# Performance work log

Hardware: AMD Instinct MI355X
Metric: run time of the kernel (lower is better)

## Reference

```python
import jax, jax.numpy as jnp
import numpy as np
import math

B, S, D = 4, 2048, 1024
H, DK, DV = 16, 64, 64
EPS = 1e-5
SCALE = math.sqrt(1.0 / D)  # NOTE: original scales by 1/sqrt(d_model), not 1/sqrt(d_k)


def setup_inputs() -> dict:
    key = jax.random.key(0)
    ks = jax.random.split(key, 12)
    s = 0.02
    return {
        "Q": jax.random.normal(ks[0], (B, S, D), jnp.float32),
        "K": jax.random.normal(ks[1], (B, S, D), jnp.float32),
        "V": jax.random.normal(ks[2], (B, S, D), jnp.float32),
        # stacked per-head projection weights (torch Linear: y = x @ W.T + b)
        "Wq": jax.random.normal(ks[3], (H, D, DK), jnp.float32) * s,
        "bq": jnp.zeros((H, DK), jnp.float32),
        "Wk": jax.random.normal(ks[4], (H, D, DK), jnp.float32) * s,
        "bk": jnp.zeros((H, DK), jnp.float32),
        "Wv": jax.random.normal(ks[5], (H, D, DV), jnp.float32) * s,
        "bv": jnp.zeros((H, DV), jnp.float32),
        "Wo": jax.random.normal(ks[6], (H * DV, D), jnp.float32) * s,
        "bo": jnp.zeros((D,), jnp.float32),
        "gamma": jnp.ones((D,), jnp.float32),
        "beta": jnp.zeros((D,), jnp.float32),
    }


def reference(Q, K, V, Wq, bq, Wk, bk, Wv, bv, Wo, bo, gamma, beta):
    residual = Q
    # batched per-head projections: [B,S,D] x [H,D,dk] -> [B,H,S,dk]
    q = jnp.einsum("bsd,hdk->bhsk", Q, Wq) + bq[None, :, None, :]
    k = jnp.einsum("bsd,hdk->bhsk", K, Wk) + bk[None, :, None, :]
    v = jnp.einsum("bsd,hdv->bhsv", V, Wv) + bv[None, :, None, :]
    # scaled dot-product attention (scale uses d_model, per original code)
    attn = jax.nn.softmax(jnp.einsum("bhsk,bhtk->bhst", q, k) * SCALE, axis=-1)
    out = jnp.einsum("bhst,bhtv->bhsv", attn, v)  # [B,H,S,DV]
    # concat heads along feature dim: [B,S,H*DV]
    out = out.transpose(0, 2, 1, 3).reshape(B, S, H * DV)
    out = out @ Wo + bo  # output projection
    # dropout is identity in eval mode
    out = out + residual
    # BatchNorm1d over (B,S) per channel (training-mode batch stats)
    mean = jnp.mean(out, axis=(0, 1))
    var = jnp.mean(jnp.square(out - mean), axis=(0, 1))
    out = (out - mean) * jax.lax.rsqrt(var + EPS) * gamma + beta
    return out.transpose(0, 2, 1)  # (B, d_model, S)
```

## Files before the change

kernel.cpp:

```cpp
#include <hip/hip_runtime.h>

#define B_ 4
#define S_ 2048
#define D_ 1024
#define H_ 16
#define SCALE_ 0.03125f
#define EPS_ 1e-5f
#define NBS_ 8192

typedef unsigned short ushort_t;
typedef __attribute__((ext_vector_type(8))) short short8;
typedef __attribute__((ext_vector_type(4))) short short4v;
typedef __attribute__((ext_vector_type(4))) float floatx4;

__device__ __forceinline__ ushort_t f2bf(float f) {
  union { float f; unsigned u; } v; v.f = f;
  unsigned r = v.u + 0x7fffu + ((v.u >> 16) & 1u);
  return (ushort_t)(r >> 16);
}

__device__ __forceinline__ float fast_exp2(float x) {
#if __has_builtin(__builtin_amdgcn_exp2f)
  return __builtin_amdgcn_exp2f(x);
#else
  return __expf(x * 0.6931471805599453f);
#endif
}

__device__ __forceinline__ short8 cvt8(float4 a, float4 b) {
  short8 r;
  r[0] = (short)f2bf(a.x); r[1] = (short)f2bf(a.y);
  r[2] = (short)f2bf(a.z); r[3] = (short)f2bf(a.w);
  r[4] = (short)f2bf(b.x); r[5] = (short)f2bf(b.y);
  r[6] = (short)f2bf(b.z); r[7] = (short)f2bf(b.w);
  return r;
}

__device__ __forceinline__ void gload16(const void* g, void* l) {
  __builtin_amdgcn_global_load_lds(
      (const __attribute__((address_space(1))) unsigned int*)g,
      (__attribute__((address_space(3))) unsigned int*)l, 16, 0, 0);
}

__global__ __launch_bounds__(256) void cvtx_k(const float* __restrict__ src,
                                              ushort_t* __restrict__ dst)
{
  size_t i = ((size_t)blockIdx.x * 256 + threadIdx.x) * 8;
  float4 a = *(const float4*)(src + i);
  float4 b = *(const float4*)(src + i + 4);
  *(short8*)(dst + i) = cvt8(a, b);
}

__global__ __launch_bounds__(256) void wtr_k(const float* __restrict__ src,
                                             ushort_t* __restrict__ dst, int mode)
{
  __shared__ float t[64][65];
  const int tr = blockIdx.x, tc = blockIdx.y;
  const float* sb; int sld;
  if (mode == 0) { sb = src + (size_t)tr * 65536 + (size_t)tc * 64 * 64; sld = 64; }
  else           { sb = src + (size_t)tc * 64 * 1024 + (size_t)tr * 64;  sld = 1024; }
  const int tid = threadIdx.x;
  const int rr = tid >> 2, cs = (tid & 3) * 16;
  const float* p = sb + (size_t)rr * sld + cs;
#pragma unroll
  for (int j = 0; j < 16; ++j) t[rr][cs + j] = p[j];
  __syncthreads();
  ushort_t* dp = dst + (size_t)(tr * 64 + rr) * 1024 + tc * 64 + cs;
#pragma unroll
  for (int j = 0; j < 16; ++j) dp[j] = f2bf(t[cs + j][rr]);
}

__global__ __launch_bounds__(256) void gemm_proj(
    const ushort_t* __restrict__ A, const ushort_t* __restrict__ Bw,
    const float* __restrict__ bias, ushort_t* __restrict__ outp, float scale)
{
  __shared__ ushort_t As[128 * 32];
  __shared__ ushort_t Bs[128 * 32];
  const int tid = threadIdx.x;
  const int wv = tid >> 6, lane = tid & 63, quad = lane >> 4, l16 = lane & 15;
  const int m0 = blockIdx.x * 128, n0 = blockIdx.y * 128;
  const int wm = wv & 1, wn = wv >> 1;
  const int lrow = lane >> 2, lkc = (lane & 3) * 8;

  floatx4 acc[4][4];
#pragma unroll
  for (int i = 0; i < 4; ++i)
#pragma unroll
    for (int j = 0; j < 4; ++j) acc[i][j] = (floatx4){0.f, 0.f, 0.f, 0.f};

  for (int k0 = 0; k0 < 1024; k0 += 32) {
    __syncthreads();
#pragma unroll
    for (int j = 0; j < 2; ++j) {
      const int rb = wv * 32 + j * 16;
      gload16(A + (size_t)(m0 + rb + lrow) * 1024 + k0 + lkc, (char*)As + rb * 64);
      gload16(Bw + (size_t)(n0 + rb + lrow) * 1024 + k0 + lkc, (char*)Bs + rb * 64);
    }
    __syncthreads();
    short8 af[4], bf[4];
#pragma unroll
    for (int i = 0; i < 4; ++i)
      af[i] = *(const short8*)&As[(wm * 64 + i * 16 + l16) * 32 + quad * 8];
#pragma unroll
    for (int i = 0; i < 4; ++i)
      bf[i] = *(const short8*)&Bs[(wn * 64 + i * 16 + l16) * 32 + quad * 8];
#pragma unroll
    for (int mi = 0; mi < 4; ++mi)
#pragma unroll
      for (int ni = 0; ni < 4; ++ni)
        acc[mi][ni] = __builtin_amdgcn_mfma_f32_16x16x32_bf16(
            af[mi], bf[ni], acc[mi][ni], 0, 0, 0);
  }

  const int b = m0 >> 11;
  const int sbase = (m0 & 2047) + wm * 64;
#pragma unroll
  for (int ni = 0; ni < 4; ++ni) {
    const int c = n0 + wn * 64 + ni * 16 + l16;
    const int h = c >> 6, nn = c & 63;
    const float bs = bias[c];
    ushort_t* op = outp + (size_t)(b * 16 + h) * 2048 * 64 + nn;
#pragma unroll
    for (int mi = 0; mi < 4; ++mi)
#pragma unroll
      for (int r = 0; r < 4; ++r) {
        int s = sbase + mi * 16 + quad * 4 + r;
        op[(size_t)s * 64] = f2bf((acc[mi][ni][r] + bs) * scale);
      }
  }
}

__global__ __launch_bounds__(256) void gemm_projT(
    const ushort_t* __restrict__ A, const ushort_t* __restrict__ Bw,
    const float* __restrict__ bias, ushort_t* __restrict__ outp)
{
  __shared__ ushort_t As[128 * 32];
  __shared__ ushort_t Bs[128 * 32];
  const int tid = threadIdx.x;
  const int wv = tid >> 6, lane = tid & 63, quad = lane >> 4, l16 = lane & 15;
  const int m0 = blockIdx.x * 128, n0 = blockIdx.y * 128;
  const int wm = wv & 1, wn = wv >> 1;
  const int lrow = lane >> 2, lkc = (lane & 3) * 8;

  floatx4 acc[4][4];
#pragma unroll
  for (int i = 0; i < 4; ++i)
#pragma unroll
    for (int j = 0; j < 4; ++j) acc[i][j] = (floatx4){0.f, 0.f, 0.f, 0.f};

  for (int k0 = 0; k0 < 1024; k0 += 32) {
    __syncthreads();
#pragma unroll
    for (int j = 0; j < 2; ++j) {
      const int rb = wv * 32 + j * 16;
      gload16(A + (size_t)(m0 + rb + lrow) * 1024 + k0 + lkc, (char*)As + rb * 64);
      gload16(Bw + (size_t)(n0 + rb + lrow) * 1024 + k0 + lkc, (char*)Bs + rb * 64);
    }
    __syncthreads();
    short8 af[4], bf[4];
#pragma unroll
    for (int i = 0; i < 4; ++i)
      af[i] = *(const short8*)&As[(wm * 64 + i * 16 + l16) * 32 + quad * 8];
#pragma unroll
    for (int i = 0; i < 4; ++i)
      bf[i] = *(const short8*)&Bs[(wn * 64 + i * 16 + l16) * 32 + quad * 8];
#pragma unroll
    for (int mi = 0; mi < 4; ++mi)
#pragma unroll
      for (int ni = 0; ni < 4; ++ni)
        acc[mi][ni] = __builtin_amdgcn_mfma_f32_16x16x32_bf16(
            af[mi], bf[ni], acc[mi][ni], 0, 0, 0);
  }

  const int b = m0 >> 11;
  const int sbase = (m0 & 2047) + wm * 64;
#pragma unroll
  for (int ni = 0; ni < 4; ++ni) {
    const int c = n0 + wn * 64 + ni * 16 + l16;
    const int h = c >> 6, nn = c & 63;
    const float bs = bias[c];
    ushort_t* op = outp + ((size_t)(b * 16 + h) * 64 + nn) * 2048;
#pragma unroll
    for (int mi = 0; mi < 4; ++mi) {
      int s0v = sbase + mi * 16 + quad * 4;
      short4v p;
#pragma unroll
      for (int r = 0; r < 4; ++r) p[r] = (short)f2bf(acc[mi][ni][r] + bs);
      *(short4v*)(op + s0v) = p;
    }
  }
}

__global__ __launch_bounds__(256) void gemm_oproj(
    const ushort_t* __restrict__ A, const ushort_t* __restrict__ Bw,
    const float* __restrict__ bo, const float* __restrict__ resid,
    float* __restrict__ y)
{
  __shared__ ushort_t As[128 * 32];
  __shared__ ushort_t Bs[128 * 32];
  const int tid = threadIdx.x;
  const int wv = tid >> 6, lane = tid & 63, quad = lane >> 4, l16 = lane & 15;
  const int m0 = blockIdx.x * 128, n0 = blockIdx.y * 128;
  const int wm = wv & 1, wn = wv >> 1;
  const int lrow = lane >> 2, lkc = (lane & 3) * 8;

  floatx4 acc[4][4];
#pragma unroll
  for (int i = 0; i < 4; ++i)
#pragma unroll
    for (int j = 0; j < 4; ++j) acc[i][j] = (floatx4){0.f, 0.f, 0.f, 0.f};

  for (int k0 = 0; k0 < 1024; k0 += 32) {
    __syncthreads();
#pragma unroll
    for (int j = 0; j < 2; ++j) {
      const int rb = wv * 32 + j * 16;
      gload16(A + (size_t)(m0 + rb + lrow) * 1024 + k0 + lkc, (char*)As + rb * 64);
      gload16(Bw + (size_t)(n0 + rb + lrow) * 1024 + k0 + lkc, (char*)Bs + rb * 64);
    }
    __syncthreads();
    short8 af[4], bf[4];
#pragma unroll
    for (int i = 0; i < 4; ++i)
      af[i] = *(const short8*)&As[(wm * 64 + i * 16 + l16) * 32 + quad * 8];
#pragma unroll
    for (int i = 0; i < 4; ++i)
      bf[i] = *(const short8*)&Bs[(wn * 64 + i * 16 + l16) * 32 + quad * 8];
#pragma unroll
    for (int mi = 0; mi < 4; ++mi)
#pragma unroll
      for (int ni = 0; ni < 4; ++ni)
        acc[mi][ni] = __builtin_amdgcn_mfma_f32_16x16x32_bf16(
            af[mi], bf[ni], acc[mi][ni], 0, 0, 0);
  }

  const int mb = m0 + wm * 64;
#pragma unroll
  for (int ni = 0; ni < 4; ++ni) {
    const int d = n0 + wn * 64 + ni * 16 + l16;
    const float bs = bo[d];
#pragma unroll
    for (int mi = 0; mi < 4; ++mi)
#pragma unroll
      for (int r = 0; r < 4; ++r) {
        int m = mb + mi * 16 + quad * 4 + r;
        y[(size_t)m * 1024 + d] = acc[mi][ni][r] + bs + resid[(size_t)m * 1024 + d];
      }
  }
}

__global__ __launch_bounds__(256, 4) void attn_k(
    const ushort_t* __restrict__ q, const ushort_t* __restrict__ k,
    const ushort_t* __restrict__ vt, ushort_t* __restrict__ ao)
{
  __shared__ ushort_t lds[20480];
  const int tid = threadIdx.x;
  const int wv = tid >> 6, lane = tid & 63, quad = lane >> 4, l16 = lane & 15;
  const int q0 = blockIdx.x * 128, h = blockIdx.y, b = blockIdx.z;
  const size_t bh = (size_t)(b * H_ + h) * S_;
  const ushort_t* vb = vt + (size_t)(b * H_ + h) * 64 * S_;

  short8 aq[2][2];
#pragma unroll
  for (int rb = 0; rb < 2; ++rb) {
    const ushort_t* qrow = q + (bh + q0 + wv * 32 + rb * 16 + l16) * 64;
    aq[rb][0] = *(const short8*)(qrow + quad * 8);
    aq[rb][1] = *(const short8*)(qrow + 32 + quad * 8);
  }

  floatx4 o[2][4];
  float ll[2][4];
#pragma unroll
  for (int rb = 0; rb < 2; ++rb) {
#pragma unroll
    for (int cb = 0; cb < 4; ++cb) o[rb][cb] = (floatx4){0.f, 0.f, 0.f, 0.f};
#pragma unroll
    for (int r = 0; r < 4; ++r) ll[rb][r] = 0.f;
  }

  const int pbase = 16384 + wv * 1024 + (l16 >> 3) * 128 + quad * 32 + (l16 & 7);

  auto stage = [&](int nb, int t0) {
#pragma unroll
    for (int i = 0; i < 4; ++i) {
      const int idx = wv * 4 + i;
      const int cb = (idx >> 1) & 3, hf = idx & 1;
      if (idx < 8)
        gload16(k + (bh + t0 + cb * 16 + l16) * 64 + hf * 32 + quad * 8,
                (char*)lds + nb * 8192 + idx * 1024);
      else
        gload16(vb + (size_t)(cb * 16 + l16) * S_ + t0 + hf * 32 + quad * 8,
                (char*)lds + 16384 + nb * 8192 + (idx - 8) * 1024);
    }
  };

  stage(0, 0);
  asm volatile("s_waitcnt vmcnt(0)" ::: "memory");
  __syncthreads();

  for (int t0 = 0; t0 < S_; t0 += 64) {
    const int nb = (t0 >> 6) & 1;
    const ushort_t* KsC = lds + nb * 4096;
    const ushort_t* VsC = lds + 8192 + nb * 4096;
    if (t0 + 64 < S_) stage(nb ^ 1, t0 + 64);

    floatx4 sc[2][4];
#pragma unroll
    for (int rb = 0; rb < 2; ++rb)
#pragma unroll
      for (int cb = 0; cb < 4; ++cb) sc[rb][cb] = (floatx4){0.f, 0.f, 0.f, 0.f};
#pragma unroll
    for (int hf = 0; hf < 2; ++hf) {
      short8 bk[4];
#pragma unroll
      for (int cb = 0; cb < 4; ++cb)
        bk[cb] = *(const short8*)&KsC[(cb * 2 + hf) * 512 + lane * 8];
#pragma unroll
      for (int rb = 0; rb < 2; ++rb)
#pragma unroll
        for (int cb = 0; cb < 4; ++cb)
          sc[rb][cb] = __builtin_amdgcn_mfma_f32_16x16x32_bf16(
              aq[rb][hf], bk[cb], sc[rb][cb], 0, 0, 0);
    }

#pragma unroll
    for (int rb = 0; rb < 2; ++rb) {
#pragma unroll
      for (int cb = 0; cb < 4; ++cb)
#pragma unroll
        for (int r = 0; r < 4; ++r) {
          float p = fast_exp2(sc[rb][cb][r]);
          ll[rb][r] += p;
          lds[pbase + (cb >> 1) * 512 + (cb & 1) * 256 + r * 8] = f2bf(p);
        }
      asm volatile("s_waitcnt lgkmcnt(0)" ::: "memory");
      __builtin_amdgcn_wave_barrier();
#pragma unroll
      for (int hf = 0; hf < 2; ++hf) {
        short8 ap = *(const short8*)&lds[16384 + wv * 1024 + hf * 512 + lane * 8];
        short8 bvf[4];
#pragma unroll
        for (int cb = 0; cb < 4; ++cb)
          bvf[cb] = *(const short8*)&VsC[(cb * 2 + hf) * 512 + lane * 8];
#pragma unroll
        for (int cb = 0; cb < 4; ++cb)
          o[rb][cb] = __builtin_amdgcn_mfma_f32_16x16x32_bf16(
              ap, bvf[cb], o[rb][cb], 0, 0, 0);
      }
      asm volatile("s_waitcnt lgkmcnt(0)" ::: "memory");
      __builtin_amdgcn_wave_barrier();
    }

    asm volatile("s_waitcnt vmcnt(0)" ::: "memory");
    __syncthreads();
  }

#pragma unroll
  for (int rb = 0; rb < 2; ++rb)
#pragma unroll
    for (int r = 0; r < 4; ++r) {
#pragma unroll
      for (int off = 8; off >= 1; off >>= 1)
        ll[rb][r] += __shfl_xor(ll[rb][r], off);
      ll[rb][r] = 1.f / ll[rb][r];
    }
#pragma unroll
  for (int rb = 0; rb < 2; ++rb)
#pragma unroll
    for (int cb = 0; cb < 4; ++cb)
#pragma unroll
      for (int r = 0; r < 4; ++r) {
        float val = o[rb][cb][r] * ll[rb][r];
        size_t idx = (size_t)(b * S_ + q0 + wv * 32 + rb * 16 + quad * 4 + r) * 1024
                     + h * 64 + cb * 16 + l16;
        ao[idx] = f2bf(val);
      }
}

__global__ __launch_bounds__(256) void stats_k(
    const float* __restrict__ y, float* __restrict__ s1, float* __restrict__ s2)
{
  const int tid = threadIdx.x;
  const int r0 = blockIdx.x * 32;
  float a[4] = {0.f, 0.f, 0.f, 0.f}, bb[4] = {0.f, 0.f, 0.f, 0.f};
  for (int r = 0; r < 32; ++r) {
    const float* row = y + (size_t)(r0 + r) * D_;
#pragma unroll
    for (int j = 0; j < 4; ++j) {
      float vv = row[tid + j * 256];
      a[j] += vv;
      bb[j] += vv * vv;
    }
  }
#pragma unroll
  for (int j = 0; j < 4; ++j) {
    atomicAdd(&s1[tid + j * 256], a[j]);
    atomicAdd(&s2[tid + j * 256], bb[j]);
  }
}

__global__ __launch_bounds__(256) void norm_k(
    const float* __restrict__ y, const float* __restrict__ s1,
    const float* __restrict__ s2, const float* __restrict__ gamma,
    const float* __restrict__ beta, float* __restrict__ out)
{
  __shared__ float tile[64][65];
  __shared__ float scl[64], sft[64];
  const int tid = threadIdx.x;
  const int s0 = blockIdx.x * 64, d0 = blockIdx.y * 64, b = blockIdx.z;

  if (tid < 64) {
    int d = d0 + tid;
    float mean = s1[d] * (1.f / (float)NBS_);
    float var = s2[d] * (1.f / (float)NBS_) - mean * mean;
    float rstd = rsqrtf(var + EPS_);
    float g = gamma[d];
    scl[tid] = rstd * g;
    sft[tid] = beta[d] - mean * rstd * g;
  }
  __syncthreads();

  const int si = tid >> 2, dc = (tid & 3) * 16;
  const float* row = y + (size_t)(b * S_ + s0 + si) * D_ + d0 + dc;
#pragma unroll
  for (int j = 0; j < 16; ++j)
    tile[si][dc + j] = row[j] * scl[dc + j] + sft[dc + j];
  __syncthreads();

  const int di = tid >> 2, sg = (tid & 3) * 16;
  float* dst = out + (size_t)(b * D_ + d0 + di) * S_ + s0 + sg;
#pragma unroll
  for (int jj = 0; jj < 4; ++jj) {
    float4 p;
    p.x = tile[sg + jj * 4 + 0][di];
    p.y = tile[sg + jj * 4 + 1][di];
    p.z = tile[sg + jj * 4 + 2][di];
    p.w = tile[sg + jj * 4 + 3][di];
    *(float4*)(dst + jj * 4) = p;
  }
}

extern "C" void kernel_launch(void* const* d_in, const int* in_sizes, int n_in,
                              void* d_out, int out_size, void* d_ws, size_t ws_size,
                              hipStream_t stream)
{
  (void)in_sizes; (void)n_in; (void)out_size; (void)ws_size;
  const float* Q     = (const float*)d_in[0];
  const float* Kin   = (const float*)d_in[1];
  const float* Vin   = (const float*)d_in[2];
  const float* Wq    = (const float*)d_in[3];
  const float* bq    = (const float*)d_in[4];
  const float* Wk    = (const float*)d_in[5];
  const float* bk    = (const float*)d_in[6];
  const float* Wv    = (const float*)d_in[7];
  const float* bv    = (const float*)d_in[8];
  const float* Wo    = (const float*)d_in[9];
  const float* bo    = (const float*)d_in[10];
  const float* gamma = (const float*)d_in[11];
  const float* beta  = (const float*)d_in[12];
  float* out = (float*)d_out;

  char* ws = (char*)d_ws;
  const size_t MB = 1u << 20;
  ushort_t* xb  = (ushort_t*)(ws);
  ushort_t* wtq = (ushort_t*)(ws + 16 * MB);
  ushort_t* wtk = (ushort_t*)(ws + 18 * MB);
  ushort_t* wtv = (ushort_t*)(ws + 20 * MB);
  ushort_t* wto = (ushort_t*)(ws + 22 * MB);
  ushort_t* qb  = (ushort_t*)(ws + 24 * MB);
  ushort_t* kb  = (ushort_t*)(ws + 40 * MB);
  ushort_t* vtb = (ushort_t*)(ws + 56 * MB);
  ushort_t* ao  = (ushort_t*)(ws);
  float*    y   = (float*)(ws + 24 * MB);
  float*    s1  = (float*)(ws + 56 * MB);
  float*    s2  = (float*)(ws + 56 * MB + 4096);

  wtr_k<<<dim3(16, 16), 256, 0, stream>>>(Wq, wtq, 0);
  wtr_k<<<dim3(16, 16), 256, 0, stream>>>(Wk, wtk, 0);
  wtr_k<<<dim3(16, 16), 256, 0, stream>>>(Wv, wtv, 0);
  wtr_k<<<dim3(16, 16), 256, 0, stream>>>(Wo, wto, 1);

  const float QSC = SCALE_ * 1.44269504088896f;
  cvtx_k<<<4096, 256, 0, stream>>>(Q, xb);
  gemm_proj<<<dim3(64, 8), 256, 0, stream>>>(xb, wtq, bq, qb, QSC);
  cvtx_k<<<4096, 256, 0, stream>>>(Kin, xb);
  gemm_proj<<<dim3(64, 8), 256, 0, stream>>>(xb, wtk, bk, kb, 1.0f);
  cvtx_k<<<4096, 256, 0, stream>>>(Vin, xb);
  gemm_projT<<<dim3(64, 8), 256, 0, stream>>>(xb, wtv, bv, vtb);

  attn_k<<<dim3(16, 16, 4), 256, 0, stream>>>(qb, kb, vtb, ao);
  gemm_oproj<<<dim3(64, 8), 256, 0, stream>>>(ao, wto, bo, Q, y);

  hipMemsetAsync(ws + 56 * MB, 0, 8192, stream);
  stats_k<<<256, 256, 0, stream>>>(y, s1, s2);
  norm_k<<<dim3(32, 16, 4), 256, 0, stream>>>(y, s1, s2, gamma, beta, out);
}
```

Measured before the change: 458.9 us.

## Transpose QK MFMA to write P as packed swizzled rows and hoist V fragment loads

The score MFMA now swaps its operands, so each lane holds four consecutive key columns of one query row. Those probabilities are packed into one 8-byte LDS store per tile, into an XOR-swizzled per-wave P buffer, instead of scattered 2-byte stores. This cuts LDS store count and bank conflicts, and makes the row sum a per-lane accumulation with a cheaper final reduction. V fragments are loaded once per tile for both row blocks, setprio is raised around the MFMA phases, and the intermediate wave barriers are removed. LDS grows and the occupancy hint drops from 4 to 3 blocks.

```diff
diff --git a/kernel.cpp b/kernel.cpp
--- a/kernel.cpp
+++ b/kernel.cpp
@@ -12,6 +12,7 @@
 typedef __attribute__((ext_vector_type(8))) short short8;
 typedef __attribute__((ext_vector_type(4))) short short4v;
 typedef __attribute__((ext_vector_type(4))) float floatx4;
+typedef __attribute__((ext_vector_type(2))) unsigned int uint2v;
 
 __device__ __forceinline__ ushort_t f2bf(float f) {
   union { float f; unsigned u; } v; v.f = f;
@@ -249,11 +250,12 @@
   }
 }
 
-__global__ __launch_bounds__(256, 4) void attn_k(
+__global__ __launch_bounds__(256, 3) void attn_k(
     const ushort_t* __restrict__ q, const ushort_t* __restrict__ k,
     const ushort_t* __restrict__ vt, ushort_t* __restrict__ ao)
 {
-  __shared__ ushort_t lds[20480];
+  __shared__ ushort_t lds[24576];
+  char* ldsb = (char*)lds;
   const int tid = threadIdx.x;
   const int wv = tid >> 6, lane = tid & 63, quad = lane >> 4, l16 = lane & 15;
   const int q0 = blockIdx.x * 128, h = blockIdx.y, b = blockIdx.z;
@@ -269,16 +271,15 @@
   }
 
   floatx4 o[2][4];
-  float ll[2][4];
-#pragma unroll
-  for (int rb = 0; rb < 2; ++rb) {
+  float ll[2] = {0.f, 0.f};
+#pragma unroll
+  for (int rb = 0; rb < 2; ++rb)
 #pragma unroll
     for (int cb = 0; cb < 4; ++cb) o[rb][cb] = (floatx4){0.f, 0.f, 0.f, 0.f};
-#pragma unroll
-    for (int r = 0; r < 4; ++r) ll[rb][r] = 0.f;
-  }
-
-  const int pbase = 16384 + wv * 1024 + (l16 >> 3) * 128 + quad * 32 + (l16 & 7);
+
+  const int swz = (l16 & 7) << 4;
+  const int q8 = quad * 8;
+  const int pb = 32768 + wv * 4096 + l16 * 128;
 
   auto stage = [&](int nb, int t0) {
 #pragma unroll
@@ -309,6 +310,7 @@
     for (int rb = 0; rb < 2; ++rb)
 #pragma unroll
       for (int cb = 0; cb < 4; ++cb) sc[rb][cb] = (floatx4){0.f, 0.f, 0.f, 0.f};
+    __builtin_amdgcn_s_setprio(1);
 #pragma unroll
     for (int hf = 0; hf < 2; ++hf) {
       short8 bk[4];
@@ -320,57 +322,71 @@
 #pragma unroll
         for (int cb = 0; cb < 4; ++cb)
           sc[rb][cb] = __builtin_amdgcn_mfma_f32_16x16x32_bf16(
-              aq[rb][hf], bk[cb], sc[rb][cb], 0, 0, 0);
-    }
+              bk[cb], aq[rb][hf], sc[rb][cb], 0, 0, 0);
+    }
+    __builtin_amdgcn_s_setprio(0);
+
+    short8 bvf[2][4];
+#pragma unroll
+    for (int hf = 0; hf < 2; ++hf)
+#pragma unroll
+      for (int cb = 0; cb < 4; ++cb)
+        bvf[hf][cb] = *(const short8*)&VsC[(cb * 2 + hf) * 512 + lane * 8];
 
 #pragma unroll
     for (int rb = 0; rb < 2; ++rb) {
 #pragma unroll
-      for (int cb = 0; cb < 4; ++cb)
-#pragma unroll
-        for (int r = 0; r < 4; ++r) {
-          float p = fast_exp2(sc[rb][cb][r]);
-          ll[rb][r] += p;
-          lds[pbase + (cb >> 1) * 512 + (cb & 1) * 256 + r * 8] = f2bf(p);
-        }
-      asm volatile("s_waitcnt lgkmcnt(0)" ::: "memory");
-      __builtin_amdgcn_wave_barrier();
+      for (int cb = 0; cb < 4; ++cb) {
+        float p0 = fast_exp2(sc[rb][cb][0]);
+        float p1 = fast_exp2(sc[rb][cb][1]);
+        float p2 = fast_exp2(sc[rb][cb][2]);
+        float p3 = fast_exp2(sc[rb][cb][3]);
+        ll[rb] += (p0 + p1) + (p2 + p3);
+        uint2v w;
+        w[0] = (unsigned)f2bf(p0) | ((unsigned)f2bf(p1) << 16);
+        w[1] = (unsigned)f2bf(p2) | ((unsigned)f2bf(p3) << 16);
+        *(uint2v*)(ldsb + pb + rb * 2048 + ((cb * 32 + q8) ^ swz)) = w;
+      }
+    }
+    asm volatile("s_waitcnt lgkmcnt(0)" ::: "memory");
+    __builtin_amdgcn_sched_barrier(0);
+
+    __builtin_amdgcn_s_setprio(1);
+#pragma unroll
+    for (int rb = 0; rb < 2; ++rb)
 #pragma unroll
       for (int hf = 0; hf < 2; ++hf) {
-        short8 ap = *(const short8*)&lds[16384 + wv * 1024 + hf * 512 + lane * 8];
-        short8 bvf[4];
-#pragma unroll
-        for (int cb = 0; cb < 4; ++cb)
-          bvf[cb] = *(const short8*)&VsC[(cb * 2 + hf) * 512 + lane * 8];
+        short8 ap = *(const short8*)(ldsb + pb + rb * 2048 +
+                                     ((hf * 64 + quad * 16) ^ swz));
 #pragma unroll
         for (int cb = 0; cb < 4; ++cb)
           o[rb][cb] = __builtin_amdgcn_mfma_f32_16x16x32_bf16(
-              ap, bvf[cb], o[rb][cb], 0, 0, 0);
+              ap, bvf[hf][cb], o[rb][cb], 0, 0, 0);
       }
-      asm volatile("s_waitcnt lgkmcnt(0)" ::: "memory");
-      __builtin_amdgcn_wave_barrier();
-    }
+    __builtin_amdgcn_s_setprio(0);
 
     asm volatile("s_waitcnt vmcnt(0)" ::: "memory");
     __syncthreads();
   }
 
 #pragma unroll
+  for (int rb = 0; rb < 2; ++rb) {
+    ll[rb] += __shfl_xor(ll[rb], 16);
+    ll[rb] += __shfl_xor(ll[rb], 32);
+  }
+  float linv[2][4];
+#pragma unroll
   for (int rb = 0; rb < 2; ++rb)
 #pragma unroll
-    for (int r = 0; r < 4; ++r) {
-#pragma unroll
-      for (int off = 8; off >= 1; off >>= 1)
-        ll[rb][r] += __shfl_xor(ll[rb][r], off);
-      ll[rb][r] = 1.f / ll[rb][r];
-    }
+    for (int r = 0; r < 4; ++r)
+      linv[rb][r] = 1.f / __shfl(ll[rb], quad * 4 + r);
 #pragma unroll
   for (int rb = 0; rb < 2; ++rb)
 #pragma unroll
     for (int cb = 0; cb < 4; ++cb)
 #pragma unroll
       for (int r = 0; r < 4; ++r) {
-        float val = o[rb][cb][r] * ll[rb][r];
+        float val = o[rb][cb][r] * linv[rb][r];
         size_t idx = (size_t)(b * S_ + q0 + wv * 32 + rb * 16 + quad * 4 + r) * 1024
                      + h * 64 + cb * 16 + l16;
         ao[idx] = f2bf(val);
```

Result: faster. 409.9 us (-10.7%).
